# Kernel optimization log

Measured on AMD Instinct MI355X. Metric: run time of the kernel, lower is better.

Reference implementation:

```python
import jax, jax.numpy as jnp
import numpy as np

INTERVAL = 0.5  # voxel_size_ratio
N_RAYS = 131072
M_SAMPLES = 8388608  # ~64 samples per ray on average
ALPHA_INIT = 0.01


def setup_inputs() -> dict:
    key = jax.random.key(0)
    k1, k2, k3 = jax.random.split(key, 3)
    density = jax.random.normal(k1, (M_SAMPLES,), jnp.float32)
    rgb_feat = jax.random.normal(k2, (M_SAMPLES, 3), jnp.float32)  # raw k0 colors
    # act_shift buffer: log(1/(1-alpha_init) - 1)
    shift = jnp.array([np.log(1.0 / (1.0 - ALPHA_INIT) - 1.0)], jnp.float32)
    # sorted ray ids (samples along each ray are contiguous, near->far)
    ray_id = jnp.sort(jax.random.randint(k3, (M_SAMPLES,), 0, N_RAYS)).astype(jnp.int32)
    return {"density": density, "rgb_feat": rgb_feat, "shift": shift,
            "ray_id": ray_id, "N": N_RAYS}


def reference(density, rgb_feat, shift, ray_id, N):
    # Raw2Alpha: alpha = 1 - (1 + exp(density + shift))^(-interval)
    #          = 1 - exp(-softplus(density + shift) * interval)
    sp = jax.nn.softplus(density + shift[0])
    log1ma = -sp * INTERVAL            # log(1 - alpha), exact
    alpha = 1.0 - jnp.exp(log1ma)

    # Alphas2Weights: per-ray exclusive cumulative product of (1 - alpha)
    # done in log space with a segmented exclusive cumsum.
    seg_tot = jax.ops.segment_sum(log1ma, ray_id, num_segments=N)   # [N] log prod per ray
    seg_excl = jnp.cumsum(seg_tot) - seg_tot                        # log prod of previous rays
    within_excl = jnp.cumsum(log1ma) - log1ma - seg_excl[ray_id]    # exclusive within segment
    T = jnp.exp(within_excl)          # transmittance before each sample
    weights = alpha * T               # [M]
    alphainv_last = jnp.exp(seg_tot)  # [N] leftover transmittance per ray

    # composite colors per ray + white-ish background via alphainv_last
    rgb = jax.nn.sigmoid(rgb_feat)
    rgb_marched = jax.ops.segment_sum(weights[:, None] * rgb, ray_id, num_segments=N)
    out = rgb_marched + alphainv_last[:, None]   # [N, 3]
    return weights, alphainv_last, out
```

## Files before the change

kernel.cpp:

```cpp
#include <hip/hip_runtime.h>


__device__ __forceinline__ float fast_sigmoid(float x) {
    return __builtin_amdgcn_rcpf(1.0f + __expf(-x));
}

struct __align__(4) f3  { float x, y, z; };
struct __align__(4) f4s { float x, y, z, w; };

#define DPP_ADD(x, ctrl, rmask)                                               \
    do {                                                                      \
        int _s = __builtin_amdgcn_update_dpp(0, __float_as_int(x), (ctrl),    \
                                             (rmask), 0xf, true);             \
        (x) += __int_as_float(_s);                                            \
    } while (0)

#define DPP_MUL(x, ctrl, rmask)                                               \
    do {                                                                      \
        int _s = __builtin_amdgcn_update_dpp(0x3f800000, __float_as_int(x),   \
                                             (ctrl), (rmask), 0xf, false);    \
        (x) *= __int_as_float(_s);                                            \
    } while (0)

__device__ __forceinline__ float half_scan_mul(float x) {
    DPP_MUL(x, 0x111, 0xf);
    DPP_MUL(x, 0x112, 0xf);
    DPP_MUL(x, 0x114, 0xf);
    DPP_MUL(x, 0x118, 0xf);
    DPP_MUL(x, 0x142, 0xa);
    return x;
}
__device__ __forceinline__ float half_scan_add(float x) {
    DPP_ADD(x, 0x111, 0xf);
    DPP_ADD(x, 0x112, 0xf);
    DPP_ADD(x, 0x114, 0xf);
    DPP_ADD(x, 0x118, 0xf);
    DPP_ADD(x, 0x142, 0xa);
    return x;
}

__device__ __forceinline__ float bperm_f(int lane, float v) {
    return __int_as_float(
        __builtin_amdgcn_ds_bpermute(lane * 4, __float_as_int(v)));
}

__global__ __launch_bounds__(256) void seg_starts4_kernel(
    const int4* __restrict__ ray4, int M4, int M, int N,
    const int* __restrict__ ray_id, int* __restrict__ starts)
{
    const int i = blockIdx.x * blockDim.x + threadIdx.x;
    if (i >= M4) return;
    const int4 v = ray4[i];
    const int prev = (i == 0) ? -1 : ray_id[4 * i - 1];
    const int base = 4 * i;
    for (int r = prev + 1; r <= v.x; ++r) starts[r] = base;
    for (int r = v.x + 1;  r <= v.y; ++r) starts[r] = base + 1;
    for (int r = v.y + 1;  r <= v.z; ++r) starts[r] = base + 2;
    for (int r = v.z + 1;  r <= v.w; ++r) starts[r] = base + 3;
    if (i == M4 - 1) {
        int last = v.w;
        for (int j = 4 * M4; j < M; ++j) {
            const int cur = ray_id[j];
            for (int r = last + 1; r <= cur; ++r) starts[r] = j;
            last = cur;
        }
        for (int r = last + 1; r <= N; ++r) starts[r] = M;
    }
}

#define RPW 2

__global__ __launch_bounds__(256, 4) void favor_render_kernel(
    const float* __restrict__ density,
    const float* __restrict__ rgb_feat,
    const float* __restrict__ shift,
    const int*   __restrict__ starts,
    int M, int N,
    float* __restrict__ weights,
    float* __restrict__ alphainv_last,
    float* __restrict__ out3)
{
    const int wave = (blockIdx.x * blockDim.x + threadIdx.x) >> 6;
    const int t    = threadIdx.x & 63;
    const int r0   = wave * RPW;
    if (r0 >= N) return;

    const int bv = starts[min(r0 + t, N)];
    const int s0 = __builtin_amdgcn_readlane(bv, 0);
    const int s1 = __builtin_amdgcn_readlane(bv, 1);
    const int s2 = __builtin_amdgcn_readlane(bv, 2);

    const int  half = t >> 5;
    const int  r    = t & 31;
    const int  st   = half ? s1 : s0;
    const int  en   = half ? s2 : s1;
    const int  len0 = s1 - s0, len1 = s2 - s1;

    const float sh = shift[0];
    const bool unsafe_tail = (s2 > M - 4);

    float carry = 1.0f, accR = 0.0f, accG = 0.0f, accB = 0.0f;
    int off = 0;

    do {
        const int i0 = st + off + 4 * r;

        float d0, d1, d2, d3;
        f3 c0, c1, c2, c3;
        if (unsafe_tail) {
            const int k0 = max(min(i0,     en - 1), 0);
            const int k1 = max(min(i0 + 1, en - 1), 0);
            const int k2 = max(min(i0 + 2, en - 1), 0);
            const int k3 = max(min(i0 + 3, en - 1), 0);
            d0 = density[k0]; d1 = density[k1];
            d2 = density[k2]; d3 = density[k3];
            c0 = *(const f3*)(rgb_feat + 3 * k0);
            c1 = *(const f3*)(rgb_feat + 3 * k1);
            c2 = *(const f3*)(rgb_feat + 3 * k2);
            c3 = *(const f3*)(rgb_feat + 3 * k3);
        } else {
            const int b  = (i0 < en) ? i0 : max(en - 4, 0);
            const f4s dv = *(const f4s*)(density + b);
            const f4s q0 = *(const f4s*)(rgb_feat + 3 * b);
            const f4s q1 = *(const f4s*)(rgb_feat + 3 * b + 4);
            const f4s q2 = *(const f4s*)(rgb_feat + 3 * b + 8);
            d0 = dv.x; d1 = dv.y; d2 = dv.z; d3 = dv.w;
            c0.x = q0.x; c0.y = q0.y; c0.z = q0.z;
            c1.x = q0.w; c1.y = q1.x; c1.z = q1.y;
            c2.x = q1.z; c2.y = q1.w; c2.z = q2.x;
            c3.x = q2.y; c3.y = q2.z; c3.z = q2.w;
        }

        const bool v0 = (i0     < en), v1 = (i0 + 1 < en);
        const bool v2 = (i0 + 2 < en), v3 = (i0 + 3 < en);

        const float u0 = 1.0f + __expf(d0 + sh);
        const float u1 = 1.0f + __expf(d1 + sh);
        const float u2 = 1.0f + __expf(d2 + sh);
        const float u3 = 1.0f + __expf(d3 + sh);
        const float a0 = v0 ? __builtin_amdgcn_rsqf(u0) : 1.0f;
        const float a1 = v1 ? __builtin_amdgcn_rsqf(u1) : 1.0f;
        const float a2 = v2 ? __builtin_amdgcn_rsqf(u2) : 1.0f;
        const float a3 = v3 ? __builtin_amdgcn_rsqf(u3) : 1.0f;

        const float m = (a0 * a1) * (a2 * a3);
        const float S = half_scan_mul(m);
        float E = bperm_f((t + 63) & 63, S);
        E = (r == 0) ? 1.0f : E;
        const float tot = bperm_f(t | 31, S);

        float p = carry * E;
        const float w0 = p * (1.0f - a0); p *= a0;
        const float w1 = p * (1.0f - a1); p *= a1;
        const float w2 = p * (1.0f - a2); p *= a2;
        const float w3 = p * (1.0f - a3);

        accR += w0 * fast_sigmoid(c0.x) + w1 * fast_sigmoid(c1.x)
              + w2 * fast_sigmoid(c2.x) + w3 * fast_sigmoid(c3.x);
        accG += w0 * fast_sigmoid(c0.y) + w1 * fast_sigmoid(c1.y)
              + w2 * fast_sigmoid(c2.y) + w3 * fast_sigmoid(c3.y);
        accB += w0 * fast_sigmoid(c0.z) + w1 * fast_sigmoid(c1.z)
              + w2 * fast_sigmoid(c2.z) + w3 * fast_sigmoid(c3.z);

        if (v3) {
            f4s wv; wv.x = w0; wv.y = w1; wv.z = w2; wv.w = w3;
            *(f4s*)(weights + i0) = wv;
        } else {
            if (v0) weights[i0]     = w0;
            if (v1) weights[i0 + 1] = w1;
            if (v2) weights[i0 + 2] = w2;
        }

        carry *= tot;
        off += 128;
    } while (len0 > off || len1 > off);

    accR = half_scan_add(accR);
    accG = half_scan_add(accG);
    accB = half_scan_add(accB);
    if ((t & 31) == 31) {
        const int ray = r0 + half;
        if (ray < N) {
            alphainv_last[ray] = carry;
            f3 o;
            o.x = accR + carry; o.y = accG + carry; o.z = accB + carry;
            *(f3*)(out3 + 3 * ray) = o;
        }
    }
}

extern "C" void kernel_launch(void* const* d_in, const int* in_sizes, int n_in,
                              void* d_out, int out_size, void* d_ws, size_t ws_size,
                              hipStream_t stream) {
    const float* density  = (const float*)d_in[0];
    const float* rgb_feat = (const float*)d_in[1];
    const float* shift    = (const float*)d_in[2];
    const int*   ray_id   = (const int*)d_in[3];

    const int M = in_sizes[0];
    const int N = (out_size - M) / 4;

    float* weights       = (float*)d_out;
    float* alphainv_last = weights + M;
    float* out3          = alphainv_last + N;

    const int block = 256;
    int* starts = (int*)d_ws;

    const int M4 = M >> 2;
    const int grid_starts = (M4 + block - 1) / block;
    seg_starts4_kernel<<<grid_starts, block, 0, stream>>>(
        (const int4*)ray_id, M4, M, N, ray_id, starts);

    const int n_waves = (N + RPW - 1) / RPW;
    const int grid_render = (n_waves * 64 + block - 1) / block;
    favor_render_kernel<<<grid_render, block, 0, stream>>>(
        density, rgb_feat, shift, starts, M, N,
        weights, alphainv_last, out3);
}
```

Baseline: 214.7 us.

## Make render waves persistent over several ray pairs with prefetch of next group

Each wave now processes up to 8 ray pairs, strided across the grid, instead of one pair. All segment starts for those pairs are loaded with a single lane-parallel read, and the first 128-sample chunk of the next pair is loaded before the current pair is computed, hiding global memory latency behind the compute. Chunks after the first fall back to clamped scalar loads and scalar weight stores. This trades register pressure and fewer resident waves for more memory-level parallelism, and the slower path for long rays may cost something.

Measured after the change: 218.1 us. Within noise of the previous version (+1.6%).

```diff
diff --git a/kernel.cpp b/kernel.cpp
--- a/kernel.cpp
+++ b/kernel.cpp
@@ -42,6 +42,9 @@
 __device__ __forceinline__ float bperm_f(int lane, float v) {
     return __int_as_float(
         __builtin_amdgcn_ds_bpermute(lane * 4, __float_as_int(v)));
+}
+__device__ __forceinline__ int rdlane(int v, int l) {
+    return __builtin_amdgcn_readlane(v, l);
 }
 
 __global__ __launch_bounds__(256) void seg_starts4_kernel(
@@ -68,7 +71,163 @@
     }
 }
 
-#define RPW 2
+#define WPB   4
+#define MAXIT 8
+
+struct Grp { float d0, d1, d2, d3; f3 c0, c1, c2, c3; };
+
+__device__ __forceinline__ Grp load_grp_f4(
+    const float* __restrict__ density, const float* __restrict__ rgb_feat,
+    int s0, int s1, int s2, int t, int M)
+{
+    const int half = t >> 5, r = t & 31;
+    const int st = half ? s1 : s0;
+    const int en = half ? s2 : s1;
+    const int i0 = st + 4 * r;
+    int b = (i0 < en) ? i0 : en - 4;
+    b = min(max(b, 0), M - 4);
+    Grp g;
+    const f4s dv = *(const f4s*)(density + b);
+    const f4s q0 = *(const f4s*)(rgb_feat + 3 * b);
+    const f4s q1 = *(const f4s*)(rgb_feat + 3 * b + 4);
+    const f4s q2 = *(const f4s*)(rgb_feat + 3 * b + 8);
+    g.d0 = dv.x; g.d1 = dv.y; g.d2 = dv.z; g.d3 = dv.w;
+    g.c0 = f3{q0.x, q0.y, q0.z};
+    g.c1 = f3{q0.w, q1.x, q1.y};
+    g.c2 = f3{q1.z, q1.w, q2.x};
+    g.c3 = f3{q2.y, q2.z, q2.w};
+    return g;
+}
+
+__device__ __forceinline__ void compute_pair(
+    const Grp& g, int s0, int s1, int s2, int t, int M, int N, int ray0,
+    float sh,
+    const float* __restrict__ density, const float* __restrict__ rgb_feat,
+    float* __restrict__ weights, float* __restrict__ alphainv_last,
+    float* __restrict__ out3)
+{
+    const int half = t >> 5, r = t & 31;
+    const int st = half ? s1 : s0;
+    const int en = half ? s2 : s1;
+    const int len0 = s1 - s0, len1 = s2 - s1;
+    const bool unsafe_tail = (s2 > M - 4);
+    const int i0 = st + 4 * r;
+
+    float d0 = g.d0, d1 = g.d1, d2 = g.d2, d3 = g.d3;
+    f3 c0 = g.c0, c1 = g.c1, c2 = g.c2, c3 = g.c3;
+    if (unsafe_tail) {
+        const int k0 = max(min(i0,     en - 1), 0);
+        const int k1 = max(min(i0 + 1, en - 1), 0);
+        const int k2 = max(min(i0 + 2, en - 1), 0);
+        const int k3 = max(min(i0 + 3, en - 1), 0);
+        d0 = density[k0]; d1 = density[k1];
+        d2 = density[k2]; d3 = density[k3];
+        c0 = *(const f3*)(rgb_feat + 3 * k0);
+        c1 = *(const f3*)(rgb_feat + 3 * k1);
+        c2 = *(const f3*)(rgb_feat + 3 * k2);
+        c3 = *(const f3*)(rgb_feat + 3 * k3);
+    }
+
+    float carry = 1.0f, accR = 0.0f, accG = 0.0f, accB = 0.0f;
+
+    {
+        const bool v0 = (i0     < en), v1 = (i0 + 1 < en);
+        const bool v2 = (i0 + 2 < en), v3 = (i0 + 3 < en);
+        const float u0 = 1.0f + __expf(d0 + sh);
+        const float u1 = 1.0f + __expf(d1 + sh);
+        const float u2 = 1.0f + __expf(d2 + sh);
+        const float u3 = 1.0f + __expf(d3 + sh);
+        const float a0 = v0 ? __builtin_amdgcn_rsqf(u0) : 1.0f;
+        const float a1 = v1 ? __builtin_amdgcn_rsqf(u1) : 1.0f;
+        const float a2 = v2 ? __builtin_amdgcn_rsqf(u2) : 1.0f;
+        const float a3 = v3 ? __builtin_amdgcn_rsqf(u3) : 1.0f;
+        const float m = (a0 * a1) * (a2 * a3);
+        const float S = half_scan_mul(m);
+        float E = bperm_f((t + 63) & 63, S);
+        E = (r == 0) ? 1.0f : E;
+        const float tot = bperm_f(t | 31, S);
+        float p = E;
+        const float w0 = p * (1.0f - a0); p *= a0;
+        const float w1 = p * (1.0f - a1); p *= a1;
+        const float w2 = p * (1.0f - a2); p *= a2;
+        const float w3 = p * (1.0f - a3);
+        accR = w0 * fast_sigmoid(c0.x) + w1 * fast_sigmoid(c1.x)
+             + w2 * fast_sigmoid(c2.x) + w3 * fast_sigmoid(c3.x);
+        accG = w0 * fast_sigmoid(c0.y) + w1 * fast_sigmoid(c1.y)
+             + w2 * fast_sigmoid(c2.y) + w3 * fast_sigmoid(c3.y);
+        accB = w0 * fast_sigmoid(c0.z) + w1 * fast_sigmoid(c1.z)
+             + w2 * fast_sigmoid(c2.z) + w3 * fast_sigmoid(c3.z);
+        if (v3) {
+            f4s wv; wv.x = w0; wv.y = w1; wv.z = w2; wv.w = w3;
+            *(f4s*)(weights + i0) = wv;
+        } else {
+            if (v0) weights[i0]     = w0;
+            if (v1) weights[i0 + 1] = w1;
+            if (v2) weights[i0 + 2] = w2;
+        }
+        carry = tot;
+    }
+
+    int off = 128;
+    while (len0 > off || len1 > off) {
+        const int ii = st + off + 4 * r;
+        const int k0 = max(min(ii,     en - 1), 0);
+        const int k1 = max(min(ii + 1, en - 1), 0);
+        const int k2 = max(min(ii + 2, en - 1), 0);
+        const int k3 = max(min(ii + 3, en - 1), 0);
+        const float e0 = density[k0], e1 = density[k1];
+        const float e2 = density[k2], e3 = density[k3];
+        const f3 x0 = *(const f3*)(rgb_feat + 3 * k0);
+        const f3 x1 = *(const f3*)(rgb_feat + 3 * k1);
+        const f3 x2 = *(const f3*)(rgb_feat + 3 * k2);
+        const f3 x3 = *(const f3*)(rgb_feat + 3 * k3);
+        const bool v0 = (ii     < en), v1 = (ii + 1 < en);
+        const bool v2 = (ii + 2 < en), v3 = (ii + 3 < en);
+        const float u0 = 1.0f + __expf(e0 + sh);
+        const float u1 = 1.0f + __expf(e1 + sh);
+        const float u2 = 1.0f + __expf(e2 + sh);
+        const float u3 = 1.0f + __expf(e3 + sh);
+        const float a0 = v0 ? __builtin_amdgcn_rsqf(u0) : 1.0f;
+        const float a1 = v1 ? __builtin_amdgcn_rsqf(u1) : 1.0f;
+        const float a2 = v2 ? __builtin_amdgcn_rsqf(u2) : 1.0f;
+        const float a3 = v3 ? __builtin_amdgcn_rsqf(u3) : 1.0f;
+        const float m = (a0 * a1) * (a2 * a3);
+        const float S = half_scan_mul(m);
+        float E = bperm_f((t + 63) & 63, S);
+        E = (r == 0) ? 1.0f : E;
+        const float tot = bperm_f(t | 31, S);
+        float p = carry * E;
+        const float w0 = p * (1.0f - a0); p *= a0;
+        const float w1 = p * (1.0f - a1); p *= a1;
+        const float w2 = p * (1.0f - a2); p *= a2;
+        const float w3 = p * (1.0f - a3);
+        accR += w0 * fast_sigmoid(x0.x) + w1 * fast_sigmoid(x1.x)
+              + w2 * fast_sigmoid(x2.x) + w3 * fast_sigmoid(x3.x);
+        accG += w0 * fast_sigmoid(x0.y) + w1 * fast_sigmoid(x1.y)
+              + w2 * fast_sigmoid(x2.y) + w3 * fast_sigmoid(x3.y);
+        accB += w0 * fast_sigmoid(x0.z) + w1 * fast_sigmoid(x1.z)
+              + w2 * fast_sigmoid(x2.z) + w3 * fast_sigmoid(x3.z);
+        if (v0) weights[ii]     = w0;
+        if (v1) weights[ii + 1] = w1;
+        if (v2) weights[ii + 2] = w2;
+        if (v3) weights[ii + 3] = w3;
+        carry *= tot;
+        off += 128;
+    }
+
+    accR = half_scan_add(accR);
+    accG = half_scan_add(accG);
+    accB = half_scan_add(accB);
+    if ((t & 31) == 31) {
+        const int ray = ray0 + half;
+        if (ray < N) {
+            alphainv_last[ray] = carry;
+            f3 o;
+            o.x = accR + carry; o.y = accG + carry; o.z = accB + carry;
+            *(f3*)(out3 + 3 * ray) = o;
+        }
+    }
+}
 
 __global__ __launch_bounds__(256, 4) void favor_render_kernel(
     const float* __restrict__ density,
@@ -80,112 +239,43 @@
     float* __restrict__ alphainv_last,
     float* __restrict__ out3)
 {
-    const int wave = (blockIdx.x * blockDim.x + threadIdx.x) >> 6;
-    const int t    = threadIdx.x & 63;
-    const int r0   = wave * RPW;
-    if (r0 >= N) return;
-
-    const int bv = starts[min(r0 + t, N)];
-    const int s0 = __builtin_amdgcn_readlane(bv, 0);
-    const int s1 = __builtin_amdgcn_readlane(bv, 1);
-    const int s2 = __builtin_amdgcn_readlane(bv, 2);
-
-    const int  half = t >> 5;
-    const int  r    = t & 31;
-    const int  st   = half ? s1 : s0;
-    const int  en   = half ? s2 : s1;
-    const int  len0 = s1 - s0, len1 = s2 - s1;
-
+    const int wid = (blockIdx.x * blockDim.x + threadIdx.x) >> 6;
+    const int t   = threadIdx.x & 63;
+    const int NW  = gridDim.x * (blockDim.x >> 6);
+
+    int bidx = N;
+    if (t < 3 * MAXIT) {
+        const int itq = t / 3, c = t - 3 * itq;
+        const int pr  = wid + itq * NW;
+        bidx = min(N, 2 * pr + c);
+    }
+    const int bv = starts[bidx];
     const float sh = shift[0];
-    const bool unsafe_tail = (s2 > M - 4);
-
-    float carry = 1.0f, accR = 0.0f, accG = 0.0f, accB = 0.0f;
-    int off = 0;
-
-    do {
-        const int i0 = st + off + 4 * r;
-
-        float d0, d1, d2, d3;
-        f3 c0, c1, c2, c3;
-        if (unsafe_tail) {
-            const int k0 = max(min(i0,     en - 1), 0);
-            const int k1 = max(min(i0 + 1, en - 1), 0);
-            const int k2 = max(min(i0 + 2, en - 1), 0);
-            const int k3 = max(min(i0 + 3, en - 1), 0);
-            d0 = density[k0]; d1 = density[k1];
-            d2 = density[k2]; d3 = density[k3];
-            c0 = *(const f3*)(rgb_feat + 3 * k0);
-            c1 = *(const f3*)(rgb_feat + 3 * k1);
-            c2 = *(const f3*)(rgb_feat + 3 * k2);
-            c3 = *(const f3*)(rgb_feat + 3 * k3);
-        } else {
-            const int b  = (i0 < en) ? i0 : max(en - 4, 0);
-            const f4s dv = *(const f4s*)(density + b);
-            const f4s q0 = *(const f4s*)(rgb_feat + 3 * b);
-            const f4s q1 = *(const f4s*)(rgb_feat + 3 * b + 4);
-            const f4s q2 = *(const f4s*)(rgb_feat + 3 * b + 8);
-            d0 = dv.x; d1 = dv.y; d2 = dv.z; d3 = dv.w;
-            c0.x = q0.x; c0.y = q0.y; c0.z = q0.z;
-            c1.x = q0.w; c1.y = q1.x; c1.z = q1.y;
-            c2.x = q1.z; c2.y = q1.w; c2.z = q2.x;
-            c3.x = q2.y; c3.y = q2.z; c3.z = q2.w;
-        }
-
-        const bool v0 = (i0     < en), v1 = (i0 + 1 < en);
-        const bool v2 = (i0 + 2 < en), v3 = (i0 + 3 < en);
-
-        const float u0 = 1.0f + __expf(d0 + sh);
-        const float u1 = 1.0f + __expf(d1 + sh);
-        const float u2 = 1.0f + __expf(d2 + sh);
-        const float u3 = 1.0f + __expf(d3 + sh);
-        const float a0 = v0 ? __builtin_amdgcn_rsqf(u0) : 1.0f;
-        const float a1 = v1 ? __builtin_amdgcn_rsqf(u1) : 1.0f;
-        const float a2 = v2 ? __builtin_amdgcn_rsqf(u2) : 1.0f;
-        const float a3 = v3 ? __builtin_amdgcn_rsqf(u3) : 1.0f;
-
-        const float m = (a0 * a1) * (a2 * a3);
-        const float S = half_scan_mul(m);
-        float E = bperm_f((t + 63) & 63, S);
-        E = (r == 0) ? 1.0f : E;
-        const float tot = bperm_f(t | 31, S);
-
-        float p = carry * E;
-        const float w0 = p * (1.0f - a0); p *= a0;
-        const float w1 = p * (1.0f - a1); p *= a1;
-        const float w2 = p * (1.0f - a2); p *= a2;
-        const float w3 = p * (1.0f - a3);
-
-        accR += w0 * fast_sigmoid(c0.x) + w1 * fast_sigmoid(c1.x)
-              + w2 * fast_sigmoid(c2.x) + w3 * fast_sigmoid(c3.x);
-        accG += w0 * fast_sigmoid(c0.y) + w1 * fast_sigmoid(c1.y)
-              + w2 * fast_sigmoid(c2.y) + w3 * fast_sigmoid(c3.y);
-        accB += w0 * fast_sigmoid(c0.z) + w1 * fast_sigmoid(c1.z)
-              + w2 * fast_sigmoid(c2.z) + w3 * fast_sigmoid(c3.z);
-
-        if (v3) {
-            f4s wv; wv.x = w0; wv.y = w1; wv.z = w2; wv.w = w3;
-            *(f4s*)(weights + i0) = wv;
-        } else {
-            if (v0) weights[i0]     = w0;
-            if (v1) weights[i0 + 1] = w1;
-            if (v2) weights[i0 + 2] = w2;
-        }
-
-        carry *= tot;
-        off += 128;
-    } while (len0 > off || len1 > off);
-
-    accR = half_scan_add(accR);
-    accG = half_scan_add(accG);
-    accB = half_scan_add(accB);
-    if ((t & 31) == 31) {
-        const int ray = r0 + half;
-        if (ray < N) {
-            alphainv_last[ray] = carry;
-            f3 o;
-            o.x = accR + carry; o.y = accG + carry; o.z = accB + carry;
-            *(f3*)(out3 + 3 * ray) = o;
-        }
+
+    Grp cur = load_grp_f4(density, rgb_feat,
+                          rdlane(bv, 0), rdlane(bv, 1), rdlane(bv, 2), t, M);
+
+    #pragma unroll
+    for (int it = 0; it < MAXIT; ++it) {
+        const int s0 = rdlane(bv, 3 * it + 0);
+        const int s1 = rdlane(bv, 3 * it + 1);
+        const int s2 = rdlane(bv, 3 * it + 2);
+        const int pr = wid + it * NW;
+
+        Grp nxt;
+        if (it + 1 < MAXIT) {
+            nxt = load_grp_f4(density, rgb_feat,
+                              rdlane(bv, 3 * it + 3),
+                              rdlane(bv, 3 * it + 4),
+                              rdlane(bv, 3 * it + 5), t, M);
+        }
+        __builtin_amdgcn_sched_barrier(0);
+
+        if (2 * pr < N) {
+            compute_pair(cur, s0, s1, s2, t, M, N, 2 * pr, sh,
+                         density, rgb_feat, weights, alphainv_last, out3);
+        }
+        cur = nxt;
     }
 }
 
@@ -212,7 +302,8 @@
     seg_starts4_kernel<<<grid_starts, block, 0, stream>>>(
         (const int4*)ray_id, M4, M, N, ray_id, starts);
 
-    const int n_waves = (N + RPW - 1) / RPW;
+    const int npairs  = (N + 1) / 2;
+    const int n_waves = (npairs + MAXIT - 1) / MAXIT;
     const int grid_render = (n_waves * 64 + block - 1) / block;
     favor_render_kernel<<<grid_render, block, 0, stream>>>(
         density, rgb_feat, shift, starts, M, N,
```
